# Optimization experiments

Hardware: AMD Instinct MI355X
Metric: run time of the kernel (lower is better)

Reference implementation:

```python
import jax, jax.numpy as jnp
import numpy as np

N, E, G = 30000, 240000, 1000
F, H = 78, 10            # in-features, GAT heads
HID = F * H              # 780
NEG_SLOPE = 0.2


def setup_inputs() -> dict:
    key = jax.random.key(0)
    ks = jax.random.split(key, 12)
    x = jax.random.normal(ks[0], (N, F), dtype=jnp.float32)
    edge_index = jax.random.randint(ks[1], (2, E), 0, N, dtype=jnp.int32)
    batch = jnp.sort(jax.random.randint(ks[2], (N,), 0, G, dtype=jnp.int32))
    def lin(k, fan_in, shape):
        return (jax.random.normal(k, shape, dtype=jnp.float32)
                / jnp.sqrt(jnp.float32(fan_in)))
    return {
        "x": x,
        "edge_index": edge_index,
        "batch": batch,
        "W_gat": lin(ks[3], F, (F, HID)),          # GATConv lin weight
        "att_src": lin(ks[4], F, (H, F)),          # GAT attention vectors
        "att_dst": lin(ks[5], F, (H, F)),
        "b_gat": jnp.zeros((HID,), jnp.float32),
        "W_gcn": lin(ks[6], HID, (HID, HID)),
        "b_gcn": jnp.zeros((HID,), jnp.float32),
        "W1": lin(ks[7], 2 * HID, (2 * HID, 1500)),
        "b1": jnp.zeros((1500,), jnp.float32),
        "W2": lin(ks[8], 1500, (1500, 128)),
        "b2": jnp.zeros((128,), jnp.float32),
    }


def _with_self_loops(edge_index):
    loop = jnp.arange(N, dtype=edge_index.dtype)
    src = jnp.concatenate([edge_index[0], loop])
    dst = jnp.concatenate([edge_index[1], loop])
    return src, dst


def reference(x, edge_index, batch, W_gat, att_src, att_dst, b_gat,
              W_gcn, b_gcn, W1, b1, W2, b2):
    src, dst = _with_self_loops(edge_index)  # [E+N]

    # ---- GATConv(78 -> 78, heads=10, concat) ----
    h = (x @ W_gat).reshape(N, H, F)                       # [N,H,F]
    a_src = jnp.einsum('nhf,hf->nh', h, att_src)           # [N,H]
    a_dst = jnp.einsum('nhf,hf->nh', h, att_dst)
    e = jax.nn.leaky_relu(a_src[src] + a_dst[dst], NEG_SLOPE)  # [Et,H]
    # segment softmax over incoming edges of each dst node
    e_max = jax.ops.segment_max(e, dst, num_segments=N)
    e_exp = jnp.exp(e - e_max[dst])
    denom = jax.ops.segment_sum(e_exp, dst, num_segments=N)
    alpha = e_exp / denom[dst]                             # [Et,H]
    msg = h[src] * alpha[:, :, None]                       # [Et,H,F]
    out = jax.ops.segment_sum(msg, dst, num_segments=N).reshape(N, HID) + b_gat
    out = jax.nn.relu(out)

    # ---- GCNConv(780 -> 780), symmetric norm with self loops ----
    h2 = out @ W_gcn                                       # [N,HID]
    deg = jax.ops.segment_sum(jnp.ones_like(dst, jnp.float32), dst,
                              num_segments=N)
    dinv = jax.lax.rsqrt(jnp.maximum(deg, 1.0))
    norm = dinv[src] * dinv[dst]                           # [Et]
    out2 = jax.ops.segment_sum(norm[:, None] * h2[src], dst,
                               num_segments=N) + b_gcn
    out2 = jax.nn.relu(out2)

    # ---- global mean / max pool over molecules ----
    counts = jax.ops.segment_sum(jnp.ones((N,), jnp.float32), batch,
                                 num_segments=G)
    gsum = jax.ops.segment_sum(out2, batch, num_segments=G)
    gmean = gsum / jnp.maximum(counts, 1.0)[:, None]
    gmax = jax.ops.segment_max(out2, batch, num_segments=G)
    gmax = jnp.where(counts[:, None] > 0, gmax, 0.0)
    pooled = jnp.concatenate([gmean, gmax], axis=1)        # [G, 1560]

    # ---- MLP head (dropout = identity at eval) ----
    hidfc = jax.nn.relu(pooled @ W1 + b1)
    return hidfc @ W2 + b2                                 # [G, 128]
```

## Files before the change

### kernel.cpp

```cpp
#include <hip/hip_runtime.h>

#define NN 30000
#define EE 240000
#define ET 270000
#define GG 1000
#define NH 10
#define FF 78
#define HID 780
#define NEG_SLOPE 0.2f

#define LD_H 784
#define KP_GCN 800
#define NP_HID 896
#define KP_X 96
#define LD_Z 960
#define MP_N 30080
#define KP_P 1600
#define NP_W1 1536
#define LD_FC 1536
#define MP_G 1024

#define MT 128
#define NT 128
#define NBLK 30
#define EB 4

#define C_X   (MP_N * KP_X)
#define C_WE  (NH * 128 * 96)
#define C_WC  (NP_HID * KP_GCN)
#define C_W1  (NP_W1 * KP_P)
#define C_W2  (128 * LD_FC)
#define C_PB  KP_GCN
#define C_WS  (FF * 2 * NH)
#define C_IN  NN
#define C_TOT (C_X + C_WE + C_WC + C_W1 + C_W2 + C_PB + C_WS + C_IN)

typedef __bf16 bf16_8 __attribute__((ext_vector_type(8)));
typedef float f32x4 __attribute__((ext_vector_type(4)));

__device__ __forceinline__ void async_copy16(const void* g, void* l) {
  __builtin_amdgcn_global_load_lds(
      (const __attribute__((address_space(1))) void*)g,
      (__attribute__((address_space(3))) void*)l, 16, 0, 0);
}

__device__ __forceinline__ float bf2f(unsigned int bits) {
  return __uint_as_float(bits << 16);
}

template <bool OUT_BF, int KBC, bool DBUF>
__global__ __launch_bounds__(256) void mfma_gemm(
    const __bf16* __restrict__ A, const __bf16* __restrict__ BT,
    float* __restrict__ Cf, __bf16* __restrict__ Cb,
    const float* __restrict__ bias, int M, int Kp, int Nout, int ldc,
    int relu, int rp, int nct, int mtiles) {
  constexpr int NST = KBC / 32;
  constexpr int TST = KBC / 16;
  constexpr int STAGEB = (KBC / 8) * MT * 8 * 2;
  __shared__ char smem[32768];
  int rt, ct;
  if (rp > 0) {
    int bid = blockIdx.x;
    int p = bid & 7, s = bid >> 3;
    int q = s / nct;
    rt = p * rp + q;
    ct = s - q * nct;
    if (rt >= mtiles) return;
  } else {
    rt = blockIdx.y; ct = blockIdx.x;
  }
  int row0 = rt * MT, col0 = ct * NT;
  int tid = threadIdx.x;
  int lane = tid & 63, wave = tid >> 6;
  int wm = (wave & 1) * 64, wn = (wave >> 1) * 64;
  int l15 = lane & 15, quad = lane >> 4;
  f32x4 acc[4][4] = {};

  auto stage = [&](int k0, int buf) {
    char* baseA = smem + (DBUF ? buf * 2 * STAGEB : 0);
    char* baseB = baseA + STAGEB;
    for (int t = 0; t < TST; t++) {
      int base = t * 256 + wave * 64;
      int s = base + lane;
      int kc = s >> 7, r = s & 127;
      async_copy16(A + (size_t)(row0 + r) * Kp + k0 + kc * 8,
                   baseA + (size_t)base * 16);
    }
    for (int t = 0; t < TST; t++) {
      int base = t * 256 + wave * 64;
      int s = base + lane;
      int kc = s >> 7, r = s & 127;
      async_copy16(BT + (size_t)(col0 + r) * Kp + k0 + kc * 8,
                   baseB + (size_t)base * 16);
    }
  };
  auto compute = [&](int buf) {
    char* baseA = smem + (DBUF ? buf * 2 * STAGEB : 0);
    char* baseB = baseA + STAGEB;
    for (int st = 0; st < NST; st++) {
      bf16_8 af[4], bfv[4];
      for (int mt = 0; mt < 4; mt++)
        af[mt] = *(const bf16_8*)(baseA +
            (size_t)((st * 4 + quad) * MT + wm + mt * 16 + l15) * 16);
      for (int nt = 0; nt < 4; nt++)
        bfv[nt] = *(const bf16_8*)(baseB +
            (size_t)((st * 4 + quad) * MT + wn + nt * 16 + l15) * 16);
      for (int mt = 0; mt < 4; mt++)
        for (int nt = 0; nt < 4; nt++)
          acc[mt][nt] = __builtin_amdgcn_mfma_f32_16x16x32_bf16(
              af[mt], bfv[nt], acc[mt][nt], 0, 0, 0);
    }
  };

  if (DBUF) {
    int niter = Kp / KBC;
    stage(0, 0);
    for (int k = 0; k < niter; k++) {
      __syncthreads();
      if (k + 1 < niter) stage((k + 1) * KBC, (k + 1) & 1);
      compute(k & 1);
    }
    __syncthreads();
  } else {
    for (int k0 = 0; k0 < Kp; k0 += KBC) {
      stage(k0, 0);
      __syncthreads();
      compute(0);
      __syncthreads();
    }
  }

  if (OUT_BF) {
    __bf16* Cs = (__bf16*)smem;
    for (int nt = 0; nt < 4; nt++) {
      int col_l = wn + nt * 16 + l15;
      int gcol = col0 + col_l;
      bool valid = gcol < Nout;
      float bv = (valid && bias) ? bias[gcol] : 0.f;
      int ch = col_l >> 3, wi = col_l & 7;
      for (int mt = 0; mt < 4; mt++) {
        for (int r = 0; r < 4; r++) {
          int rl = wm + mt * 16 + quad * 4 + r;
          float v = 0.f;
          if (valid) {
            v = acc[mt][nt][r] + bv;
            if (relu) v = fmaxf(v, 0.f);
          }
          Cs[rl * 128 + ((ch ^ (rl & 7)) << 3) + wi] = (__bf16)v;
        }
      }
    }
    __syncthreads();
    for (int idx = tid; idx < MT * 16; idx += 256) {
      int rl = idx >> 4, ch = idx & 15;
      int grow = row0 + rl, gcol = col0 + ch * 8;
      if (grow < M && gcol + 8 <= ldc)
        *(bf16_8*)(Cb + (size_t)grow * ldc + gcol) =
            *(const bf16_8*)&Cs[rl * 128 + ((ch ^ (rl & 7)) << 3)];
    }
  } else {
    for (int nt = 0; nt < 4; nt++) {
      int col = col0 + wn + nt * 16 + l15;
      if (col >= ldc) continue;
      bool valid = col < Nout;
      float bv = (valid && bias) ? bias[col] : 0.f;
      for (int mt = 0; mt < 4; mt++) {
        int rbase = row0 + wm + mt * 16 + quad * 4;
        for (int r = 0; r < 4; r++) {
          int row = rbase + r;
          if (row >= M) continue;
          float v = 0.f;
          if (valid) {
            v = acc[mt][nt][r] + bv;
            if (relu) v = fmaxf(v, 0.f);
          }
          Cf[(size_t)row * ldc + col] = v;
        }
      }
    }
  }
}

__global__ __launch_bounds__(256) void gemm_head(
    const __bf16* __restrict__ z, const __bf16* __restrict__ WE,
    const float* __restrict__ pb, __bf16* __restrict__ C) {
  __shared__ char smem[49152];
  __bf16* As = (__bf16*)smem;
  __bf16* Bs = (__bf16*)(smem + 24576);
  int head = blockIdx.x;
  int row0 = blockIdx.y * MT;
  int col0 = 80 * head;
  int tid = threadIdx.x;
  int lane = tid & 63, wave = tid >> 6;
  int wm = (wave & 1) * 64, wn = (wave >> 1) * 64;
  int l15 = lane & 15, quad = lane >> 4;

  for (int t = 0; t < 6; t++) {
    int base = t * 256 + wave * 64;
    int s = base + lane;
    int kc = s >> 7, r = s & 127;
    async_copy16(z + (size_t)(row0 + r) * LD_Z + 96 * head + kc * 8,
                 (char*)As + (size_t)base * 16);
  }
  for (int t = 0; t < 6; t++) {
    int base = t * 256 + wave * 64;
    int s = base + lane;
    int kc = s >> 7, r = s & 127;
    async_copy16(WE + (size_t)head * 128 * 96 + (size_t)r * 96 + kc * 8,
                 (char*)Bs + (size_t)base * 16);
  }
  __syncthreads();

  f32x4 acc[4][4] = {};
  for (int st = 0; st < 3; st++) {
    bf16_8 af[4], bfv[4];
    for (int mt = 0; mt < 4; mt++)
      af[mt] = *(const bf16_8*)&As[(size_t)((st * 4 + quad) * 128 + wm + mt * 16 + l15) * 8];
    for (int nt = 0; nt < 4; nt++)
      bfv[nt] = *(const bf16_8*)&Bs[(size_t)((st * 4 + quad) * 128 + wn + nt * 16 + l15) * 8];
    for (int mt = 0; mt < 4; mt++)
      for (int nt = 0; nt < 4; nt++)
        acc[mt][nt] = __builtin_amdgcn_mfma_f32_16x16x32_bf16(
            af[mt], bfv[nt], acc[mt][nt], 0, 0, 0);
  }
  __syncthreads();

  __bf16* Cs = (__bf16*)smem;
  for (int nt = 0; nt < 4; nt++) {
    int col_l = wn + nt * 16 + l15;
    bool valid = col_l < 78;
    float bv = valid ? pb[col0 + col_l] : 0.f;
    int ch = col_l >> 3, wi = col_l & 7;
    for (int mt = 0; mt < 4; mt++) {
      for (int r = 0; r < 4; r++) {
        int rl = wm + mt * 16 + quad * 4 + r;
        float v = valid ? fmaxf(acc[mt][nt][r] + bv, 0.f) : 0.f;
        Cs[rl * 128 + ((ch ^ (rl & 7)) << 3) + wi] = (__bf16)v;
      }
    }
  }
  __syncthreads();
  for (int idx = tid; idx < MT * 10; idx += 256) {
    int rl = idx / 10, ch = idx - rl * 10;
    int grow = row0 + rl;
    if (grow < NN)
      *(bf16_8*)(C + (size_t)grow * KP_GCN + col0 + ch * 8) =
          *(const bf16_8*)&Cs[rl * 128 + ((ch ^ (rl & 7)) << 3)];
  }
}

__global__ __launch_bounds__(256) void prep_kernel(
    const float* __restrict__ x, const float* __restrict__ W_gat,
    const float* __restrict__ att_src, const float* __restrict__ att_dst,
    const float* __restrict__ W_gcn, const float* __restrict__ W1,
    const float* __restrict__ W2, const float* __restrict__ b_gat,
    __bf16* __restrict__ x_bf, __bf16* __restrict__ WE,
    __bf16* __restrict__ WgcnT, __bf16* __restrict__ W1T,
    __bf16* __restrict__ W2T, float* __restrict__ pb,
    float* __restrict__ wsd, int* __restrict__ cnt, int* __restrict__ fill,
    int* __restrict__ lo, int* __restrict__ hi) {
  int gid = blockIdx.x * 256 + threadIdx.x;
  if (gid < C_X) {
    int n = gid / KP_X, k = gid - n * KP_X;
    x_bf[gid] = (__bf16)((n < NN && k < FF) ? x[(size_t)n * FF + k] : 0.f);
    return;
  }
  gid -= C_X;
  if (gid < C_WE) {
    int h = gid / (128 * 96);
    int rem = gid - h * 128 * 96;
    int n = rem / 96, k = rem - n * 96;
    WE[gid] = (__bf16)((n < FF && k < FF)
                           ? W_gat[(size_t)k * HID + h * FF + n] : 0.f);
    return;
  }
  gid -= C_WE;
  if (gid < C_WC) {
    int n = gid / KP_GCN, kp = gid - n * KP_GCN;
    int hh = kp / 80, f = kp - hh * 80;
    WgcnT[gid] = (__bf16)((n < HID && f < FF)
                              ? W_gcn[(size_t)(FF * hh + f) * HID + n] : 0.f);
    return;
  }
  gid -= C_WC;
  if (gid < C_W1) {
    int n = gid / KP_P, k = gid - n * KP_P;
    W1T[gid] = (__bf16)((n < 1500 && k < 2 * HID) ? W1[(size_t)k * 1500 + n] : 0.f);
    return;
  }
  gid -= C_W1;
  if (gid < C_W2) {
    int n = gid / LD_FC, k = gid - n * LD_FC;
    W2T[gid] = (__bf16)((n < 128 && k < 1500) ? W2[(size_t)k * 128 + n] : 0.f);
    return;
  }
  gid -= C_W2;
  if (gid < C_PB) {
    int hh = gid / 80, f = gid - hh * 80;
    pb[gid] = (f < FF) ? b_gat[FF * hh + f] : 0.f;
    return;
  }
  gid -= C_PB;
  if (gid < C_WS) {
    int k = gid / (2 * NH), c = gid - k * (2 * NH);
    int h = (c < NH) ? c : c - NH;
    const float* att = (c < NH) ? att_src : att_dst;
    float s = 0.f;
    for (int f = 0; f < FF; f++)
      s += W_gat[(size_t)k * HID + h * FF + f] * att[h * FF + f];
    wsd[k * 2 * NH + c] = s;
    return;
  }
  gid -= C_WS;
  if (gid < C_IN) {
    cnt[gid] = 0; fill[gid] = 0;
    if (gid < GG) { lo[gid] = NN; hi[gid] = 0; }
  }
}

__device__ __forceinline__ void edge_sd(const int* __restrict__ ei, int t,
                                        int& s, int& d) {
  if (t < EE) { s = ei[t]; d = ei[EE + t]; }
  else        { s = t - EE; d = t - EE; }
}

__global__ __launch_bounds__(256) void adot_count_kernel(
    const float* __restrict__ x, const float* __restrict__ wsd,
    float* __restrict__ a_src, float* __restrict__ a_dst,
    const int* __restrict__ ei, const int* __restrict__ batch,
    int* __restrict__ cnt, int* __restrict__ lo, int* __restrict__ hi) {
  __shared__ float w_s[FF * 2 * NH];
  for (int i = threadIdx.x; i < FF * 2 * NH; i += 256) w_s[i] = wsd[i];
  int gid = blockIdx.x * 256 + threadIdx.x;
  if (gid < ET) { int s, d; edge_sd(ei, gid, s, d); atomicAdd(&cnt[d], 1); }
  if (gid < NN) {
    int g = batch[gid];
    atomicMin(&lo[g], gid);
    atomicMax(&hi[g], gid + 1);
  }
  __syncthreads();
  if (gid >= NN * 2 * NH) return;
  int n = gid / (2 * NH), c = gid - n * (2 * NH);
  float s = 0.f;
  for (int k = 0; k < FF; k++) s += x[(size_t)n * FF + k] * w_s[k * 2 * NH + c];
  if (c < NH) a_src[n * NH + c] = s;
  else        a_dst[n * NH + (c - NH)] = s;
}

__global__ __launch_bounds__(1024) void scan1_kernel(
    const int* __restrict__ cnt, int* __restrict__ row_ptr,
    int* __restrict__ partial) {
  __shared__ int buf[1024];
  int i = blockIdx.x * 1024 + threadIdx.x;
  int v = (i < NN) ? cnt[i] : 0;
  buf[threadIdx.x] = v;
  __syncthreads();
  for (int off = 1; off < 1024; off <<= 1) {
    int t = (threadIdx.x >= off) ? buf[threadIdx.x - off] : 0;
    __syncthreads();
    buf[threadIdx.x] += t;
    __syncthreads();
  }
  if (i < NN) row_ptr[i] = buf[threadIdx.x] - v;
  if (threadIdx.x == 1023) partial[blockIdx.x] = buf[1023];
}

__global__ __launch_bounds__(256) void scan3_kernel(
    int* __restrict__ row_ptr, const int* __restrict__ partial,
    const int* __restrict__ cnt, float* __restrict__ dinv) {
  __shared__ int pre[NBLK];
  if (threadIdx.x == 0) {
    int run = 0;
    for (int b = 0; b < NBLK; b++) { pre[b] = run; run += partial[b]; }
  }
  __syncthreads();
  int i = blockIdx.x * 256 + threadIdx.x;
  if (i < NN) {
    row_ptr[i] += pre[i >> 10];
    dinv[i] = rsqrtf((float)max(cnt[i], 1));
  }
  if (i == 0) row_ptr[NN] = ET;
}

__global__ void scatter_kernel(const int* __restrict__ ei,
                               const int* __restrict__ row_ptr,
                               int* __restrict__ fill,
                               const float* __restrict__ a_src,
                               const float* __restrict__ a_dst,
                               int* __restrict__ col_src,
                               float* __restrict__ p_csr) {
  int t = blockIdx.x * blockDim.x + threadIdx.x;
  if (t >= ET) return;
  int s, d; edge_sd(ei, t, s, d);
  int pos = row_ptr[d] + atomicAdd(&fill[d], 1);
  col_src[pos] = s;
#pragma unroll
  for (int h = 0; h < NH; h++) {
    float v = a_src[s * NH + h] + a_dst[d * NH + h];
    v = (v > 0.f) ? v : v * NEG_SLOPE;
    p_csr[(size_t)pos * NH + h] = __expf(v);
  }
}

__global__ __launch_bounds__(256) void gat_x_aggr_kernel(
    const int* __restrict__ row_ptr, const int* __restrict__ col_src,
    const float* __restrict__ p_csr, const __bf16* __restrict__ x_bf,
    __bf16* __restrict__ z) {
  int wave = threadIdx.x >> 6;
  int lane = threadIdx.x & 63;
  int d = blockIdx.x * 2 + (wave >> 1);
  int idx = (wave & 1) * 64 + lane;
  int beg = row_ptr[d], end = row_ptr[d + 1];

  if (idx < 100) {
    int h = idx / 10, j = idx - h * 10;
    int k0 = 8 * j;
    float acc[8] = {};
    float sum = 0.f;
    for (int e = beg; e < end; e += EB) {
      int sidx[EB]; float pp[EB];
#pragma unroll
      for (int q = 0; q < EB; q++) {
        bool ok = (e + q < end);
        int ee = ok ? e + q : beg;
        sidx[q] = col_src[ee];
        float p = p_csr[(size_t)ee * NH + h];
        pp[q] = ok ? p : 0.f;
      }
      uint4 rr[EB];
#pragma unroll
      for (int q = 0; q < EB; q++)
        rr[q] = *(const uint4*)(x_bf + (size_t)sidx[q] * KP_X + k0);
#pragma unroll
      for (int q = 0; q < EB; q++) {
        sum += pp[q];
        unsigned int w[4] = {rr[q].x, rr[q].y, rr[q].z, rr[q].w};
#pragma unroll
        for (int k = 0; k < 8; k++) {
          unsigned int bits = (k & 1) ? (w[k >> 1] >> 16) : (w[k >> 1] & 0xffffu);
          acc[k] += bf2f(bits) * pp[q];
        }
      }
    }
    float inv = 1.f / sum;
    bf16_8 o;
#pragma unroll
    for (int k = 0; k < 8; k++) {
      float val = (k0 + k < FF) ? acc[k] * inv : 0.f;
      o[k] = (__bf16)val;
    }
    *(bf16_8*)(z + (size_t)d * LD_Z + 96 * h + k0) = o;
  } else if (idx < 120) {
    int t = idx - 100;
    int h = t >> 1;
    int k0 = 80 + 8 * (t & 1);
    bf16_8 zz = {};
    *(bf16_8*)(z + (size_t)d * LD_Z + 96 * h + k0) = zz;
  }
}

__global__ __launch_bounds__(256) void gcn_aggr_kernel(
    const int* __restrict__ row_ptr, const int* __restrict__ col_src,
    const float* __restrict__ dinv, const __bf16* __restrict__ h2,
    const float* __restrict__ b_gcn, __bf16* __restrict__ out2) {
  int wave = threadIdx.x >> 6;
  int lane = threadIdx.x & 63;
  int d = blockIdx.x * 2 + (wave >> 1);
  int half = wave & 1;
  int beg = row_ptr[d], end = row_ptr[d + 1];
  if (lane >= 49) return;
  int f0 = half * 392 + 8 * lane;
  float dv = dinv[d];
  float acc[8] = {};
  for (int e = beg; e < end; e += EB) {
    int sidx[EB]; float ww[EB];
#pragma unroll
    for (int j = 0; j < EB; j++) {
      bool ok = (e + j < end);
      int ee = ok ? e + j : beg;
      int s = col_src[ee];
      sidx[j] = s;
      ww[j] = ok ? dinv[s] * dv : 0.f;
    }
    uint4 rr[EB];
#pragma unroll
    for (int j = 0; j < EB; j++)
      rr[j] = *(const uint4*)(h2 + (size_t)sidx[j] * LD_H + f0);
#pragma unroll
    for (int j = 0; j < EB; j++) {
      unsigned int wb[4] = {rr[j].x, rr[j].y, rr[j].z, rr[j].w};
#pragma unroll
      for (int k = 0; k < 8; k++) {
        unsigned int bits = (k & 1) ? (wb[k >> 1] >> 16) : (wb[k >> 1] & 0xffffu);
        acc[k] += bf2f(bits) * ww[j];
      }
    }
  }
  bf16_8 o0;
#pragma unroll
  for (int k = 0; k < 8; k++) {
    int f = f0 + k;
    float val = (f < HID) ? fmaxf(acc[k] + b_gcn[f], 0.f) : 0.f;
    o0[k] = (__bf16)val;
  }
  *(bf16_8*)(out2 + (size_t)d * LD_H + f0) = o0;
}

__global__ __launch_bounds__(128) void pool_kernel(
    const __bf16* __restrict__ out2, const int* __restrict__ lo,
    const int* __restrict__ hi, __bf16* __restrict__ pooled) {
  int g = blockIdx.x;
  int l = lo[g], h = hi[g];
  int t = threadIdx.x;
  if (t >= 98) {
    if (t < 103) {
      int base = 1560 + (t - 98) * 8;
      for (int k = 0; k < 8; k++) pooled[(size_t)g * KP_P + base + k] = (__bf16)0.f;
    }
    return;
  }
  int f0 = 8 * t;
  float s[8] = {}, mx[8];
#pragma unroll
  for (int k = 0; k < 8; k++) mx[k] = -1e30f;
  for (int n = l; n < h; n++) {
    uint4 r = *(const uint4*)(out2 + (size_t)n * LD_H + f0);
    unsigned int w[4] = {r.x, r.y, r.z, r.w};
#pragma unroll
    for (int k = 0; k < 8; k++) {
      unsigned int bits = (k & 1) ? (w[k >> 1] >> 16) : (w[k >> 1] & 0xffffu);
      float v = bf2f(bits);
      s[k] += v;
      mx[k] = fmaxf(mx[k], v);
    }
  }
  float invc = (h > l) ? 1.f / (float)(h - l) : 0.f;
#pragma unroll
  for (int k = 0; k < 8; k++) {
    int f = f0 + k;
    if (f >= HID) continue;
    float mean = (h > l) ? s[k] * invc : 0.f;
    float mxx  = (h > l) ? mx[k] : 0.f;
    pooled[(size_t)g * KP_P + f] = (__bf16)mean;
    pooled[(size_t)g * KP_P + HID + f] = (__bf16)mxx;
  }
}

extern "C" void kernel_launch(void* const* d_in, const int* in_sizes, int n_in,
                              void* d_out, int out_size, void* d_ws,
                              size_t ws_size, hipStream_t stream) {
  const float* x        = (const float*)d_in[0];
  const int*   edge_idx = (const int*)d_in[1];
  const int*   batch    = (const int*)d_in[2];
  const float* W_gat    = (const float*)d_in[3];
  const float* att_src  = (const float*)d_in[4];
  const float* att_dst  = (const float*)d_in[5];
  const float* b_gat    = (const float*)d_in[6];
  const float* W_gcn    = (const float*)d_in[7];
  const float* b_gcn    = (const float*)d_in[8];
  const float* W1       = (const float*)d_in[9];
  const float* b1       = (const float*)d_in[10];
  const float* W2       = (const float*)d_in[11];
  const float* b2       = (const float*)d_in[12];
  float* out = (float*)d_out;
  (void)in_sizes; (void)n_in; (void)out_size; (void)ws_size;

  char* ws = (char*)d_ws;
  size_t off = 0;
  auto alloc = [&](size_t bytes) -> void* {
    void* p = ws + off;
    off += (bytes + 255) & ~(size_t)255;
    return p;
  };
  char*  bufR     = (char*)alloc((size_t)MP_N * KP_GCN * 2);
  __bf16* A_bf    = (__bf16*)bufR;
  __bf16* out2b   = (__bf16*)bufR;
  __bf16* z_bf    = (__bf16*)alloc((size_t)MP_N * LD_Z * 2);
  __bf16* h2_bf   = (__bf16*)alloc((size_t)MP_N * LD_H * 2);
  __bf16* x_bf    = (__bf16*)alloc((size_t)MP_N * KP_X * 2);
  __bf16* WE      = (__bf16*)alloc((size_t)NH * 128 * 96 * 2);
  __bf16* WgcnT   = (__bf16*)alloc((size_t)NP_HID * KP_GCN * 2);
  __bf16* W1T     = (__bf16*)alloc((size_t)NP_W1 * KP_P * 2);
  __bf16* W2T     = (__bf16*)alloc((size_t)128 * LD_FC * 2);
  __bf16* pooled  = (__bf16*)alloc((size_t)MP_G * KP_P * 2);
  __bf16* hidfc   = (__bf16*)alloc((size_t)MP_G * LD_FC * 2);
  float* pb       = (float*)alloc((size_t)KP_GCN * 4);
  float* wsd      = (float*)alloc((size_t)FF * 2 * NH * 4);
  float* a_src_b  = (float*)alloc((size_t)NN * NH * 4);
  float* a_dst_b  = (float*)alloc((size_t)NN * NH * 4);
  float* p_csr    = (float*)alloc((size_t)ET * NH * 4);
  int*   cnt      = (int*)alloc((size_t)NN * 4);
  int*   fill     = (int*)alloc((size_t)NN * 4);
  int*   row_ptr  = (int*)alloc((size_t)(NN + 1) * 4);
  int*   col_src  = (int*)alloc((size_t)ET * 4);
  int*   partial  = (int*)alloc((size_t)NBLK * 4);
  int*   lo       = (int*)alloc((size_t)GG * 4);
  int*   hi       = (int*)alloc((size_t)GG * 4);
  float* dinv     = (float*)alloc((size_t)NN * 4);

  prep_kernel<<<(C_TOT + 255) / 256, 256, 0, stream>>>(
      x, W_gat, att_src, att_dst, W_gcn, W1, W2, b_gat, x_bf, WE, WgcnT, W1T,
      W2T, pb, wsd, cnt, fill, lo, hi);

  adot_count_kernel<<<(NN * 2 * NH + 255) / 256, 256, 0, stream>>>(
      x, wsd, a_src_b, a_dst_b, edge_idx, batch, cnt, lo, hi);

  scan1_kernel<<<NBLK, 1024, 0, stream>>>(cnt, row_ptr, partial);
  scan3_kernel<<<(NN + 255) / 256, 256, 0, stream>>>(row_ptr, partial, cnt,
                                                     dinv);
  scatter_kernel<<<(ET + 255) / 256, 256, 0, stream>>>(
      edge_idx, row_ptr, fill, a_src_b, a_dst_b, col_src, p_csr);

  gat_x_aggr_kernel<<<NN / 2, 256, 0, stream>>>(row_ptr, col_src, p_csr, x_bf,
                                                z_bf);
  gemm_head<<<dim3(NH, MP_N / MT), 256, 0, stream>>>(z_bf, WE, pb, A_bf);
  {
    mfma_gemm<true, 32, true><<<dim3(8 * 30 * 7), 256, 0, stream>>>(
        A_bf, WgcnT, nullptr, h2_bf, nullptr, NN, KP_GCN, HID, LD_H, 0,
        30, 7, MP_N / MT);
  }
  gcn_aggr_kernel<<<NN / 2, 256, 0, stream>>>(row_ptr, col_src, dinv, h2_bf,
                                              b_gcn, out2b);

  pool_kernel<<<GG, 128, 0, stream>>>(out2b, lo, hi, pooled);

  {
    dim3 grid(NP_W1 / NT, MP_G / MT);
    mfma_gemm<true, 64, false><<<grid, 256, 0, stream>>>(
        pooled, W1T, nullptr, hidfc, b1, GG, KP_P, 1500, LD_FC, 1, 0, 0, 0);
  }
  {
    dim3 grid(1, MP_G / MT);
    mfma_gemm<false, 64, false><<<grid, 256, 0, stream>>>(
        hidfc, W2T, out, nullptr, b2, GG, LD_FC, 128, 128, 0, 0, 0, 0);
  }
}
```

Measured before the change: 537.3 us.

## Split edge scatter from exp, widen GCN gather batch, double-buffer MLP GEMMs

The scatter kernel now writes only col_src and a new dst_csr array. A separate pexp_kernel computes the attention exponentials in CSR order, so p_csr is written with coalesced stores instead of scattered ones. The GCN aggregation gathers 6 neighbour rows per iteration instead of 4 for more memory-level parallelism, and the two MLP GEMMs switch to the double-buffered variant, with shared memory sized to fit. The cost is an extra kernel launch, an extra ET-sized int array, higher register pressure in the gather loop, and more LDS per block in the MLP GEMMs.

Measured after the change: 523.7 us, median of 3. 2.5% less time.

```diff
diff --git a/kernel.cpp b/kernel.cpp
--- a/kernel.cpp
+++ b/kernel.cpp
@@ -24,6 +24,7 @@
 #define NT 128
 #define NBLK 30
 #define EB 4
+#define EBG 6
 
 #define C_X   (MP_N * KP_X)
 #define C_WE  (NH * 128 * 96)
@@ -57,7 +58,9 @@
   constexpr int NST = KBC / 32;
   constexpr int TST = KBC / 16;
   constexpr int STAGEB = (KBC / 8) * MT * 8 * 2;
-  __shared__ char smem[32768];
+  constexpr int NEED = (DBUF ? 4 : 2) * STAGEB;
+  constexpr int SMEM = NEED > 32768 ? NEED : 32768;
+  __shared__ char smem[SMEM];
   int rt, ct;
   if (rp > 0) {
     int bid = blockIdx.x;
@@ -385,20 +388,29 @@
 __global__ void scatter_kernel(const int* __restrict__ ei,
                                const int* __restrict__ row_ptr,
                                int* __restrict__ fill,
-                               const float* __restrict__ a_src,
-                               const float* __restrict__ a_dst,
                                int* __restrict__ col_src,
-                               float* __restrict__ p_csr) {
+                               int* __restrict__ dst_csr) {
   int t = blockIdx.x * blockDim.x + threadIdx.x;
   if (t >= ET) return;
   int s, d; edge_sd(ei, t, s, d);
   int pos = row_ptr[d] + atomicAdd(&fill[d], 1);
   col_src[pos] = s;
+  dst_csr[pos] = d;
+}
+
+__global__ void pexp_kernel(const int* __restrict__ col_src,
+                            const int* __restrict__ dst_csr,
+                            const float* __restrict__ a_src,
+                            const float* __restrict__ a_dst,
+                            float* __restrict__ p_csr) {
+  int t = blockIdx.x * blockDim.x + threadIdx.x;
+  if (t >= ET) return;
+  int s = col_src[t], d = dst_csr[t];
 #pragma unroll
   for (int h = 0; h < NH; h++) {
     float v = a_src[s * NH + h] + a_dst[d * NH + h];
     v = (v > 0.f) ? v : v * NEG_SLOPE;
-    p_csr[(size_t)pos * NH + h] = __expf(v);
+    p_csr[(size_t)t * NH + h] = __expf(v);
   }
 }
 
@@ -472,22 +484,22 @@
   int f0 = half * 392 + 8 * lane;
   float dv = dinv[d];
   float acc[8] = {};
-  for (int e = beg; e < end; e += EB) {
-    int sidx[EB]; float ww[EB];
-#pragma unroll
-    for (int j = 0; j < EB; j++) {
+  for (int e = beg; e < end; e += EBG) {
+    int sidx[EBG]; float ww[EBG];
+#pragma unroll
+    for (int j = 0; j < EBG; j++) {
       bool ok = (e + j < end);
       int ee = ok ? e + j : beg;
       int s = col_src[ee];
       sidx[j] = s;
       ww[j] = ok ? dinv[s] * dv : 0.f;
     }
-    uint4 rr[EB];
-#pragma unroll
-    for (int j = 0; j < EB; j++)
+    uint4 rr[EBG];
+#pragma unroll
+    for (int j = 0; j < EBG; j++)
       rr[j] = *(const uint4*)(h2 + (size_t)sidx[j] * LD_H + f0);
 #pragma unroll
-    for (int j = 0; j < EB; j++) {
+    for (int j = 0; j < EBG; j++) {
       unsigned int wb[4] = {rr[j].x, rr[j].y, rr[j].z, rr[j].w};
 #pragma unroll
       for (int k = 0; k < 8; k++) {
@@ -593,6 +605,7 @@
   int*   fill     = (int*)alloc((size_t)NN * 4);
   int*   row_ptr  = (int*)alloc((size_t)(NN + 1) * 4);
   int*   col_src  = (int*)alloc((size_t)ET * 4);
+  int*   dst_csr  = (int*)alloc((size_t)ET * 4);
   int*   partial  = (int*)alloc((size_t)NBLK * 4);
   int*   lo       = (int*)alloc((size_t)GG * 4);
   int*   hi       = (int*)alloc((size_t)GG * 4);
@@ -608,8 +621,10 @@
   scan1_kernel<<<NBLK, 1024, 0, stream>>>(cnt, row_ptr, partial);
   scan3_kernel<<<(NN + 255) / 256, 256, 0, stream>>>(row_ptr, partial, cnt,
                                                      dinv);
-  scatter_kernel<<<(ET + 255) / 256, 256, 0, stream>>>(
-      edge_idx, row_ptr, fill, a_src_b, a_dst_b, col_src, p_csr);
+  scatter_kernel<<<(ET + 255) / 256, 256, 0, stream>>>(edge_idx, row_ptr,
+                                                       fill, col_src, dst_csr);
+  pexp_kernel<<<(ET + 255) / 256, 256, 0, stream>>>(col_src, dst_csr,
+                                                    a_src_b, a_dst_b, p_csr);
 
   gat_x_aggr_kernel<<<NN / 2, 256, 0, stream>>>(row_ptr, col_src, p_csr, x_bf,
                                                 z_bf);
@@ -626,12 +641,12 @@
 
   {
     dim3 grid(NP_W1 / NT, MP_G / MT);
-    mfma_gemm<true, 64, false><<<grid, 256, 0, stream>>>(
+    mfma_gemm<true, 64, true><<<grid, 256, 0, stream>>>(
         pooled, W1T, nullptr, hidfc, b1, GG, KP_P, 1500, LD_FC, 1, 0, 0, 0);
   }
   {
     dim3 grid(1, MP_G / MT);
-    mfma_gemm<false, 64, false><<<grid, 256, 0, stream>>>(
+    mfma_gemm<false, 64, true><<<grid, 256, 0, stream>>>(
         hidfc, W2T, out, nullptr, b2, GG, LD_FC, 128, 128, 0, 0, 0, 0);
   }
 }
```
